# Kernel optimization log

Hardware: AMD Instinct MI355X
Metric: run time of the kernel (lower is better)

The kernel has to match this reference:

```python
import jax, jax.numpy as jnp
import numpy as np

B, S, H, GLU, VOC, L, CIN, BLK = 8, 256, 512, 1024, 256, 24, 320, 16
EPS = 1e-5


def setup_inputs() -> dict:
    key = jax.random.key(0)
    ks = jax.random.split(key, 16)
    r = lambda k, shp, s=0.02: (jax.random.normal(k, shp) * s).astype(jnp.float32)
    return {
        "x": jax.random.normal(ks[0], (B, CIN, 1, S), dtype=jnp.float32),
        "stem_w": r(ks[1], (H, CIN)),
        "rms_local": jnp.ones((L, H), jnp.float32),
        "rms_global": jnp.ones((L, H), jnp.float32),
        "rms_ffn": jnp.ones((L, H), jnp.float32),
        # alphas init to 0.0 in the torch module; use small nonzero values so
        # all sublayers actually contribute to the output / gradients.
        "alpha_local": (jax.random.normal(ks[2], (L,)) * 0.1).astype(jnp.float32),
        "alpha_global": (jax.random.normal(ks[3], (L,)) * 0.1).astype(jnp.float32),
        "alpha_mlp": (jax.random.normal(ks[4], (L,)) * 0.1).astype(jnp.float32),
        "w_local": r(ks[5], (L, H, BLK, BLK), 0.06),   # per-channel 16x16 mixing mats
        "w_global": r(ks[6], (L, H, BLK, BLK), 0.06),
        "wv": r(ks[7], (L, GLU, H)),
        "wg": r(ks[8], (L, GLU, H)),
        "wo": r(ks[9], (L, H, GLU)),
        "head_rms": jnp.ones((H,), jnp.float32),
        "head_logit_scale": jnp.float32(1.0),
        "head_w": r(ks[10], (VOC, H)),
    }


def _rmsnorm(h, w):
    # h: [B,C,S], w: [C]; mean-of-squares over channel axis (C == HIDDEN == 512)
    ms = jnp.mean(h * h, axis=1, keepdims=True)
    return h * jax.lax.rsqrt(ms + EPS) * w[None, :, None]


def _forward(x, stem_w, rms_local, rms_global, rms_ffn, alpha_local, alpha_global,
             alpha_mlp, w_local, w_global, wv, wg, wo, head_rms, head_logit_scale, head_w):
    h = jnp.einsum('oc,bcs->bos', stem_w, x[:, :, 0, :])  # stem conv1x1 -> [B,H,S]
    params = (rms_local, rms_global, rms_ffn, alpha_local, alpha_global, alpha_mlp,
              w_local, w_global, wv, wg, wo)

    def step(h, p):
        rl, rg, rf, al, ag, am, Wl, Wg, Wv, Wgt, Wo = p
        # s = i*16 + j : i = chunk index, j = within-chunk position
        u = _rmsnorm(h, rl).reshape(B, H, BLK, BLK)
        h = h + al * jnp.einsum('cpj,bcij->bcip', Wl, u).reshape(B, H, S)   # local: mix j
        v = _rmsnorm(h, rg).reshape(B, H, BLK, BLK)
        h = h + ag * jnp.einsum('cpi,bcij->bcpj', Wg, v).reshape(B, H, S)   # global: mix i
        w_ = _rmsnorm(h, rf)
        h1 = jnp.einsum('oc,bcs->bos', Wv, w_)
        h3 = jnp.einsum('oc,bcs->bos', Wgt, w_)
        h = h + am * jnp.einsum('co,bos->bcs', Wo, jax.nn.silu(h1) * h3)    # GLU MLP
        return h, None

    h, _ = jax.lax.scan(step, h, params)
    n = _rmsnorm(h, head_rms)
    logits = head_logit_scale * jnp.einsum('vc,bcs->bvs', head_w, n)
    return logits[:, :, None, :]  # [B, VOCAB, 1, S]


def reference(x, stem_w, rms_local, rms_global, rms_ffn, alpha_local, alpha_global,
              alpha_mlp, w_local, w_global, wv, wg, wo, head_rms, head_logit_scale, head_w):
    return _forward(x, stem_w, rms_local, rms_global, rms_ffn, alpha_local, alpha_global,
                    alpha_mlp, w_local, w_global, wv, wg, wo, head_rms,
                    head_logit_scale, head_w)
```

## Files before the change

kernel.cpp:

```cpp
#include <hip/hip_runtime.h>
#include <hip/hip_bf16.h>
#include <stdint.h>

#define NB 8
#define NS 256
#define NH 512
#define NG 1024
#define NV 256
#define NL 24
#define NC 320
#define NT 2048
#define EPSF 1e-5f

typedef __bf16 bf16;
typedef bf16 bf16x8 __attribute__((ext_vector_type(8)));
typedef float f32x4 __attribute__((ext_vector_type(4)));

__device__ __forceinline__ bf16 f2bf(float f) {
    uint32_t u = __builtin_bit_cast(uint32_t, f);
    u += 0x7FFFu + ((u >> 16) & 1u);
    uint16_t b = (uint16_t)(u >> 16);
    return __builtin_bit_cast(bf16, b);
}
__device__ __forceinline__ uint16_t bfbits(float f) {
    uint32_t u = __builtin_bit_cast(uint32_t, f);
    u += 0x7FFFu + ((u >> 16) & 1u);
    return (uint16_t)(u >> 16);
}

__device__ __forceinline__ void gload16(const void* g, void* l) {
    __builtin_amdgcn_global_load_lds(
        (const __attribute__((address_space(1))) void*)g,
        (__attribute__((address_space(3))) void*)l,
        16, 0, 0);
}

__device__ __forceinline__ void stage64(
    const bf16* __restrict__ src, int ldk, bf16* lds, int wv_, int lane)
{
    #pragma unroll
    for (int j = 0; j < 2; ++j) {
        const int gI = wv_*2 + j;
        const int r  = gI*8 + (lane >> 3);
        const int ch = (lane & 7) ^ (lane >> 3);
        gload16(src + (size_t)r*ldk + ch*8, lds + gI*512);
    }
}
__device__ __forceinline__ const bf16x8* fragp(const bf16* lds, int row, int ch) {
    return (const bf16x8*)(lds + row*64 + ((ch ^ (row & 7)) << 3));
}

#define MFMA(a,b,c) __builtin_amdgcn_mfma_f32_16x16x32_bf16(a, b, c, 0, 0, 0)

__global__ __launch_bounds__(256) void k_cvt(
    const float* __restrict__ src, bf16* __restrict__ dst, int n8)
{
    int i = blockIdx.x*256 + threadIdx.x;
    const int stride = gridDim.x*256;
    for (; i < n8; i += stride) {
        const float* sp = src + (size_t)i*8;
        float4 v0 = *(const float4*)&sp[0];
        float4 v1 = *(const float4*)&sp[4];
        bf16x8 t;
        t[0] = f2bf(v0.x); t[1] = f2bf(v0.y); t[2] = f2bf(v0.z); t[3] = f2bf(v0.w);
        t[4] = f2bf(v1.x); t[5] = f2bf(v1.y); t[6] = f2bf(v1.z); t[7] = f2bf(v1.w);
        *(bf16x8*)&dst[(size_t)i*8] = t;
    }
}

__global__ __launch_bounds__(256) void k_cvt2(
    const float* __restrict__ s0, const float* __restrict__ s1,
    bf16* __restrict__ d0, bf16* __restrict__ d1, int n8a, int n8b)
{
    const int N = n8a + n8b;
    for (int i = blockIdx.x*256 + threadIdx.x; i < N; i += gridDim.x*256) {
        const float* s; bf16* d; int j;
        if (i < n8a) { s = s0; d = d0; j = i; }
        else         { s = s1; d = d1; j = i - n8a; }
        const float* sp = s + (size_t)j*8;
        float4 v0 = *(const float4*)&sp[0];
        float4 v1 = *(const float4*)&sp[4];
        bf16x8 t;
        t[0] = f2bf(v0.x); t[1] = f2bf(v0.y); t[2] = f2bf(v0.z); t[3] = f2bf(v0.w);
        t[4] = f2bf(v1.x); t[5] = f2bf(v1.y); t[6] = f2bf(v1.z); t[7] = f2bf(v1.w);
        *(bf16x8*)&d[(size_t)j*8] = t;
    }
}

__global__ __launch_bounds__(256) void k_trw(
    const float* __restrict__ wl, const float* __restrict__ wg,
    bf16* __restrict__ wlT, bf16* __restrict__ wgT)
{
    __shared__ bf16 Ls[64*72];
    const int pj0 = blockIdx.x*64, c0 = blockIdx.y*64;
    const int z = blockIdx.z, l = z >> 1;
    const float* src = (z & 1) ? wg : wl;
    bf16* dst = (z & 1) ? wgT : wlT;
    src += (size_t)l*NH*256;
    dst += (size_t)l*256*NH;
    const int tid = threadIdx.x;
    #pragma unroll
    for (int e = 0; e < 16; ++e) {
        int idx = e*256 + tid;
        int cl = idx >> 6, pj = idx & 63;
        Ls[pj*72 + cl] = f2bf(src[(size_t)(c0 + cl)*256 + pj0 + pj]);
    }
    __syncthreads();
    #pragma unroll
    for (int e = 0; e < 2; ++e) {
        int idx = e*256 + tid;
        int row = idx >> 3, ch8 = idx & 7;
        *(bf16x8*)&dst[(size_t)(pj0 + row)*NH + c0 + ch8*8] =
            *(const bf16x8*)&Ls[row*72 + ch8*8];
    }
}

__global__ __launch_bounds__(256) void k_trx(
    const float* __restrict__ x, bf16* __restrict__ xT)
{
    __shared__ bf16 Ls[64*72];
    const int s0 = blockIdx.x*64, c0 = blockIdx.y*64, b = blockIdx.z;
    const int tid = threadIdx.x;
    #pragma unroll
    for (int e = 0; e < 16; ++e) {
        int idx = tid + e*256;
        int c = idx >> 6, s = idx & 63;
        Ls[s*72 + c] = f2bf(x[(size_t)(b*NC + c0 + c)*NS + s0 + s]);
    }
    __syncthreads();
    #pragma unroll
    for (int e = 0; e < 2; ++e) {
        int idx = tid + e*256;
        int s = idx >> 3, ch = idx & 7;
        *(bf16x8*)&xT[(size_t)(b*NS + s0 + s)*NC + c0 + ch*8] =
            *(const bf16x8*)&Ls[s*72 + ch*8];
    }
}

__global__ __launch_bounds__(256) void k_stem_b(
    const bf16* __restrict__ xT, const bf16* __restrict__ wb,
    float* __restrict__ h)
{
    __shared__ __align__(16) bf16 As[2][4096], Bs[2][4096];
    __shared__ float Cs[64*66];
    const int t0 = blockIdx.x*64, n0 = blockIdx.y*64;
    const int tid = threadIdx.x, lane = tid & 63, wv_ = tid >> 6;
    const int wm = wv_ >> 1, wn = wv_ & 1;
    const int fr = lane & 15, kq = lane >> 4;
    const bf16* Ag = xT + (size_t)t0*NC;
    const bf16* Bg = wb + (size_t)n0*NC;
    f32x4 acc[2][2] = {};
    stage64(Ag, NC, As[0], wv_, lane);
    stage64(Bg, NC, Bs[0], wv_, lane);
    __syncthreads();
    const int NIT = NC/64;
    for (int it = 0; it < NIT; ++it) {
        const int cur = it & 1;
        if (it + 1 < NIT) {
            stage64(Ag + (it+1)*64, NC, As[cur^1], wv_, lane);
            stage64(Bg + (it+1)*64, NC, Bs[cur^1], wv_, lane);
        }
        #pragma unroll
        for (int kk = 0; kk < 2; ++kk) {
            const int ch = kk*4 + kq;
            bf16x8 a0 = *fragp(As[cur], wm*32 + fr,      ch);
            bf16x8 a1 = *fragp(As[cur], wm*32 + 16 + fr, ch);
            bf16x8 b0 = *fragp(Bs[cur], wn*32 + fr,      ch);
            bf16x8 b1 = *fragp(Bs[cur], wn*32 + 16 + fr, ch);
            acc[0][0] = MFMA(a0, b0, acc[0][0]);
            acc[0][1] = MFMA(a0, b1, acc[0][1]);
            acc[1][0] = MFMA(a1, b0, acc[1][0]);
            acc[1][1] = MFMA(a1, b1, acc[1][1]);
        }
        __syncthreads();
    }
    const int row4 = (lane >> 4)*4, col = lane & 15;
    #pragma unroll
    for (int mi = 0; mi < 2; ++mi)
      #pragma unroll
      for (int ni = 0; ni < 2; ++ni)
        #pragma unroll
        for (int r = 0; r < 4; ++r)
            Cs[(wm*32 + mi*16 + row4 + r)*66 + wn*32 + ni*16 + col] = acc[mi][ni][r];
    __syncthreads();
    const int rr = tid >> 2, c16 = (tid & 3)*16;
    float* dst = &h[(size_t)(t0 + rr)*NH + n0 + c16];
    #pragma unroll
    for (int i = 0; i < 16; ++i) dst[i] = Cs[rr*66 + c16 + i];
}

template<int STR, bool FFN>
__global__ __launch_bounds__(256) void k_mix2(
    float* __restrict__ h, const bf16* __restrict__ wT,
    const float* __restrict__ rmsw, const float* __restrict__ alpha_p,
    const float* __restrict__ rmsw_ffn, bf16* __restrict__ a_bf)
{
    __shared__ float raw[16][512];
    __shared__ float red[4][16];
    __shared__ float rstdL[16];
    const int b = blockIdx.x, gi = blockIdx.y, ph = blockIdx.z;
    const int base = b*NS + (STR == 1 ? gi*16 : gi);
    const int tid = threadIdx.x, lane = tid & 63, wid = tid >> 6;
    #pragma unroll
    for (int e = 0; e < 8; ++e) {
        int idx = e*256 + tid;
        int k = idx >> 7, c4 = idx & 127;
        *(float4*)&raw[k][c4*4] = *(const float4*)&h[(size_t)(base + k*STR)*NH + c4*4];
    }
    __syncthreads();
    const int c0 = tid*2;
    float u0[16], u1[16], part[16];
    #pragma unroll
    for (int k = 0; k < 16; ++k) {
        float A = raw[k][c0], B = raw[k][c0+1];
        u0[k] = A; u1[k] = B; part[k] = A*A + B*B;
    }
    #pragma unroll
    for (int m = 1; m < 64; m <<= 1)
        #pragma unroll
        for (int k = 0; k < 16; ++k) part[k] += __shfl_xor(part[k], m, 64);
    if (lane == 0) {
        #pragma unroll
        for (int k = 0; k < 16; ++k) red[wid][k] = part[k];
    }
    __syncthreads();
    if (tid < 16)
        rstdL[tid] = rsqrtf((red[0][tid]+red[1][tid]+red[2][tid]+red[3][tid])*(1.f/NH) + EPSF);
    __syncthreads();
    #pragma unroll
    for (int k = 0; k < 16; ++k) { u0[k] *= rstdL[k]; u1[k] *= rstdL[k]; }
    const float al = *alpha_p;
    const float rc0 = rmsw[c0]*al, rc1 = rmsw[c0+1]*al;
    const uint32_t* wrow = (const uint32_t*)wT + tid;
    float hn0[8], hn1[8];
    #pragma unroll
    for (int pp = 0; pp < 8; ++pp) {
        const int p = ph*8 + pp;
        float a0 = 0.f, a1 = 0.f;
        #pragma unroll
        for (int k = 0; k < 16; ++k) {
            uint32_t wz = wrow[(p*16 + k)*256];
            float w0 = __builtin_bit_cast(float, wz << 16);
            float w1 = __builtin_bit_cast(float, wz & 0xffff0000u);
            a0 += w0*u0[k]; a1 += w1*u1[k];
        }
        hn0[pp] = raw[p][c0]   + rc0*a0;
        hn1[pp] = raw[p][c0+1] + rc1*a1;
        float2 o; o.x = hn0[pp]; o.y = hn1[pp];
        *(float2*)&h[(size_t)(base + p*STR)*NH + c0] = o;
    }
    if constexpr (FFN) {
        float p2[8];
        #pragma unroll
        for (int pp = 0; pp < 8; ++pp) p2[pp] = hn0[pp]*hn0[pp] + hn1[pp]*hn1[pp];
        #pragma unroll
        for (int m = 1; m < 64; m <<= 1)
            #pragma unroll
            for (int pp = 0; pp < 8; ++pp) p2[pp] += __shfl_xor(p2[pp], m, 64);
        __syncthreads();
        if (lane == 0) {
            #pragma unroll
            for (int pp = 0; pp < 8; ++pp) red[wid][pp] = p2[pp];
        }
        __syncthreads();
        if (tid < 8)
            rstdL[tid] = rsqrtf((red[0][tid]+red[1][tid]+red[2][tid]+red[3][tid])*(1.f/NH) + EPSF);
        __syncthreads();
        const float rf0 = rmsw_ffn[c0], rf1 = rmsw_ffn[c0+1];
        #pragma unroll
        for (int pp = 0; pp < 8; ++pp) {
            const int p = ph*8 + pp;
            float r = rstdL[pp];
            uint32_t pk = ((uint32_t)bfbits(hn1[pp]*r*rf1) << 16) | bfbits(hn0[pp]*r*rf0);
            *(uint32_t*)&a_bf[(size_t)(base + p*STR)*NH + c0] = pk;
        }
    }
}

__global__ __launch_bounds__(256) void k_norm2(
    const float* __restrict__ h, const float* __restrict__ rmsw,
    bf16* __restrict__ a)
{
    const int t = blockIdx.x*4 + (threadIdx.x >> 6);
    const int lane = threadIdx.x & 63;
    const int c8 = lane*8;
    const float* src = &h[(size_t)t*NH + c8];
    float4 h0 = *(const float4*)&src[0];
    float4 h1 = *(const float4*)&src[4];
    float ss = h0.x*h0.x + h0.y*h0.y + h0.z*h0.z + h0.w*h0.w
             + h1.x*h1.x + h1.y*h1.y + h1.z*h1.z + h1.w*h1.w;
    #pragma unroll
    for (int m = 1; m < 64; m <<= 1) ss += __shfl_xor(ss, m, 64);
    const float rstd = rsqrtf(ss*(1.f/NH) + EPSF);
    float4 w0 = *(const float4*)&rmsw[c8];
    float4 w1 = *(const float4*)&rmsw[c8 + 4];
    bf16x8 o;
    o[0] = f2bf(h0.x*rstd*w0.x); o[1] = f2bf(h0.y*rstd*w0.y);
    o[2] = f2bf(h0.z*rstd*w0.z); o[3] = f2bf(h0.w*rstd*w0.w);
    o[4] = f2bf(h1.x*rstd*w1.x); o[5] = f2bf(h1.y*rstd*w1.y);
    o[6] = f2bf(h1.z*rstd*w1.z); o[7] = f2bf(h1.w*rstd*w1.w);
    *(bf16x8*)&a[(size_t)t*NH + c8] = o;
}

__global__ __launch_bounds__(256) void k_mlp_in(
    const bf16* __restrict__ a, const bf16* __restrict__ wvl,
    const bf16* __restrict__ wgl, bf16* __restrict__ g)
{
    __shared__ __align__(16) bf16 As[2][4096], B1s[2][4096], B3s[2][4096];
    __shared__ bf16 Gs[64*72];
    const int t0 = blockIdx.x*64, n0 = blockIdx.y*64;
    const int tid = threadIdx.x, lane = tid & 63, wv_ = tid >> 6;
    const int wm = wv_ >> 1, wn = wv_ & 1;
    const int fr = lane & 15, kq = lane >> 4;
    const bf16* Ag = a   + (size_t)t0*NH;
    const bf16* Vg = wvl + (size_t)n0*NH;
    const bf16* Gg = wgl + (size_t)n0*NH;
    f32x4 acc1[2][2] = {}, acc3[2][2] = {};
    stage64(Ag, NH, As[0],  wv_, lane);
    stage64(Vg, NH, B1s[0], wv_, lane);
    stage64(Gg, NH, B3s[0], wv_, lane);
    __syncthreads();
    const int NIT = NH/64;
    for (int it = 0; it < NIT; ++it) {
        const int cur = it & 1;
        if (it + 1 < NIT) {
            stage64(Ag + (it+1)*64, NH, As[cur^1],  wv_, lane);
            stage64(Vg + (it+1)*64, NH, B1s[cur^1], wv_, lane);
            stage64(Gg + (it+1)*64, NH, B3s[cur^1], wv_, lane);
        }
        #pragma unroll
        for (int kk = 0; kk < 2; ++kk) {
            const int ch = kk*4 + kq;
            bf16x8 a0 = *fragp(As[cur],  wm*32 + fr,      ch);
            bf16x8 a1 = *fragp(As[cur],  wm*32 + 16 + fr, ch);
            bf16x8 u0 = *fragp(B1s[cur], wn*32 + fr,      ch);
            bf16x8 u1 = *fragp(B1s[cur], wn*32 + 16 + fr, ch);
            bf16x8 v0 = *fragp(B3s[cur], wn*32 + fr,      ch);
            bf16x8 v1 = *fragp(B3s[cur], wn*32 + 16 + fr, ch);
            acc1[0][0] = MFMA(a0, u0, acc1[0][0]);
            acc1[0][1] = MFMA(a0, u1, acc1[0][1]);
            acc1[1][0] = MFMA(a1, u0, acc1[1][0]);
            acc1[1][1] = MFMA(a1, u1, acc1[1][1]);
            acc3[0][0] = MFMA(a0, v0, acc3[0][0]);
            acc3[0][1] = MFMA(a0, v1, acc3[0][1]);
            acc3[1][0] = MFMA(a1, v0, acc3[1][0]);
            acc3[1][1] = MFMA(a1, v1, acc3[1][1]);
        }
        __syncthreads();
    }
    const int row4 = (lane >> 4)*4, col = lane & 15;
    #pragma unroll
    for (int mi = 0; mi < 2; ++mi)
      #pragma unroll
      for (int ni = 0; ni < 2; ++ni)
        #pragma unroll
        for (int r = 0; r < 4; ++r) {
            float xv = acc1[mi][ni][r];
            float gl = (xv / (1.f + __expf(-xv))) * acc3[mi][ni][r];
            Gs[(wm*32 + mi*16 + row4 + r)*72 + wn*32 + ni*16 + col] = f2bf(gl);
        }
    __syncthreads();
    const int rr = tid >> 2, c16 = (tid & 3)*16;
    bf16x8 o0 = *(const bf16x8*)&Gs[rr*72 + c16];
    bf16x8 o1 = *(const bf16x8*)&Gs[rr*72 + c16 + 8];
    *(bf16x8*)&g[(size_t)(t0 + rr)*NG + n0 + c16] = o0;
    *(bf16x8*)&g[(size_t)(t0 + rr)*NG + n0 + c16 + 8] = o1;
}

__global__ __launch_bounds__(256) void k_mlp_out(
    const bf16* __restrict__ g, const bf16* __restrict__ wol,
    const float* __restrict__ alpha_p, float* __restrict__ h)
{
    __shared__ __align__(16) bf16 As[2][4096], Bs[2][4096];
    __shared__ float Cs[64*66];
    const int t0 = blockIdx.x*64, n0 = blockIdx.y*64;
    const int tid = threadIdx.x, lane = tid & 63, wv_ = tid >> 6;
    const int wm = wv_ >> 1, wn = wv_ & 1;
    const int fr = lane & 15, kq = lane >> 4;
    const bf16* Ag = g   + (size_t)t0*NG;
    const bf16* Bg = wol + (size_t)n0*NG;
    f32x4 acc[2][2] = {};
    stage64(Ag, NG, As[0], wv_, lane);
    stage64(Bg, NG, Bs[0], wv_, lane);
    __syncthreads();
    const int NIT = NG/64;
    for (int it = 0; it < NIT; ++it) {
        const int cur = it & 1;
        if (it + 1 < NIT) {
            stage64(Ag + (it+1)*64, NG, As[cur^1], wv_, lane);
            stage64(Bg + (it+1)*64, NG, Bs[cur^1], wv_, lane);
        }
        #pragma unroll
        for (int kk = 0; kk < 2; ++kk) {
            const int ch = kk*4 + kq;
            bf16x8 a0 = *fragp(As[cur], wm*32 + fr,      ch);
            bf16x8 a1 = *fragp(As[cur], wm*32 + 16 + fr, ch);
            bf16x8 b0 = *fragp(Bs[cur], wn*32 + fr,      ch);
            bf16x8 b1 = *fragp(Bs[cur], wn*32 + 16 + fr, ch);
            acc[0][0] = MFMA(a0, b0, acc[0][0]);
            acc[0][1] = MFMA(a0, b1, acc[0][1]);
            acc[1][0] = MFMA(a1, b0, acc[1][0]);
            acc[1][1] = MFMA(a1, b1, acc[1][1]);
        }
        __syncthreads();
    }
    const int row4 = (lane >> 4)*4, col = lane & 15;
    #pragma unroll
    for (int mi = 0; mi < 2; ++mi)
      #pragma unroll
      for (int ni = 0; ni < 2; ++ni)
        #pragma unroll
        for (int r = 0; r < 4; ++r)
            Cs[(wm*32 + mi*16 + row4 + r)*66 + wn*32 + ni*16 + col] = acc[mi][ni][r];
    __syncthreads();
    const float am = *alpha_p;
    const int rr = tid >> 2, c16 = (tid & 3)*16;
    float* dst = &h[(size_t)(t0 + rr)*NH + n0 + c16];
    #pragma unroll
    for (int i = 0; i < 16; ++i)
        dst[i] = dst[i] + am * Cs[rr*66 + c16 + i];
}

__global__ __launch_bounds__(256) void k_head(
    const bf16* __restrict__ a, const bf16* __restrict__ hw,
    const float* __restrict__ scale_p, float* __restrict__ out)
{
    __shared__ __align__(16) bf16 As[2][4096], Bs[2][4096];
    __shared__ float Ls[64*66];
    const int t0 = blockIdx.x*64, n0 = blockIdx.y*64;
    const int tid = threadIdx.x, lane = tid & 63, wv_ = tid >> 6;
    const int wm = wv_ >> 1, wn = wv_ & 1;
    const int fr = lane & 15, kq = lane >> 4;
    const bf16* Ag = a  + (size_t)t0*NH;
    const bf16* Bg = hw + (size_t)n0*NH;
    f32x4 acc[2][2] = {};
    stage64(Ag, NH, As[0], wv_, lane);
    stage64(Bg, NH, Bs[0], wv_, lane);
    __syncthreads();
    const int NIT = NH/64;
    for (int it = 0; it < NIT; ++it) {
        const int cur = it & 1;
        if (it + 1 < NIT) {
            stage64(Ag + (it+1)*64, NH, As[cur^1], wv_, lane);
            stage64(Bg + (it+1)*64, NH, Bs[cur^1], wv_, lane);
        }
        #pragma unroll
        for (int kk = 0; kk < 2; ++kk) {
            const int ch = kk*4 + kq;
            bf16x8 a0 = *fragp(As[cur], wm*32 + fr,      ch);
            bf16x8 a1 = *fragp(As[cur], wm*32 + 16 + fr, ch);
            bf16x8 b0 = *fragp(Bs[cur], wn*32 + fr,      ch);
            bf16x8 b1 = *fragp(Bs[cur], wn*32 + 16 + fr, ch);
            acc[0][0] = MFMA(a0, b0, acc[0][0]);
            acc[0][1] = MFMA(a0, b1, acc[0][1]);
            acc[1][0] = MFMA(a1, b0, acc[1][0]);
            acc[1][1] = MFMA(a1, b1, acc[1][1]);
        }
        __syncthreads();
    }
    const float sc = *scale_p;
    const int row4 = (lane >> 4)*4, col = lane & 15;
    #pragma unroll
    for (int mi = 0; mi < 2; ++mi)
      #pragma unroll
      for (int ni = 0; ni < 2; ++ni)
        #pragma unroll
        for (int r = 0; r < 4; ++r)
            Ls[(wm*32 + mi*16 + row4 + r)*66 + wn*32 + ni*16 + col] = sc * acc[mi][ni][r];
    __syncthreads();
    const int vv = tid >> 2, s16 = (tid & 3)*16;
    const int b = t0 >> 8, s0 = t0 & 255;
    float* dst = &out[((size_t)(b*NV + n0 + vv))*NS + s0 + s16];
    #pragma unroll
    for (int i = 0; i < 16; ++i) dst[i] = Ls[(s16 + i)*66 + vv];
}

extern "C" void kernel_launch(void* const* d_in, const int* in_sizes, int n_in,
                              void* d_out, int out_size, void* d_ws, size_t ws_size,
                              hipStream_t stream) {
    const float* x          = (const float*)d_in[0];
    const float* stem_w     = (const float*)d_in[1];
    const float* rms_local  = (const float*)d_in[2];
    const float* rms_global = (const float*)d_in[3];
    const float* rms_ffn    = (const float*)d_in[4];
    const float* alpha_local  = (const float*)d_in[5];
    const float* alpha_global = (const float*)d_in[6];
    const float* alpha_mlp    = (const float*)d_in[7];
    const float* w_local    = (const float*)d_in[8];
    const float* w_global   = (const float*)d_in[9];
    const float* wv         = (const float*)d_in[10];
    const float* wg         = (const float*)d_in[11];
    const float* wo         = (const float*)d_in[12];
    const float* head_rms   = (const float*)d_in[13];
    const float* head_scale = (const float*)d_in[14];
    const float* head_w     = (const float*)d_in[15];
    float* out = (float*)d_out;

    char* ws = (char*)d_ws;
    const size_t MB = 1024*1024;
    float* h    = (float*)(ws);
    bf16*  g    = (bf16*)(ws + 4*MB);
    bf16*  a_bf = (bf16*)(ws + 8*MB);
    bf16* xT      = (bf16*)(ws + 16*MB);
    bf16* stem_wb = (bf16*)(ws + 18*MB);
    bf16* head_wb = (bf16*)(ws + 19*MB);
    bf16* wlT     = (bf16*)(ws + 20*MB);
    bf16* wgT     = (bf16*)(ws + 26*MB);
    bf16* wv_b    = (bf16*)(ws + 32*MB);
    bf16* wg_b    = (bf16*)(ws + 56*MB);
    bf16* wo_b    = (bf16*)(ws + 80*MB);

    k_cvt<<<2048, 256, 0, stream>>>(wv, wv_b, NL*NG*NH/8);
    k_cvt<<<2048, 256, 0, stream>>>(wg, wg_b, NL*NG*NH/8);
    k_cvt<<<2048, 256, 0, stream>>>(wo, wo_b, NL*NH*NG/8);
    k_cvt2<<<160, 256, 0, stream>>>(stem_w, head_w, stem_wb, head_wb,
                                    NH*NC/8, NV*NH/8);
    k_trw<<<dim3(4, 8, 48), 256, 0, stream>>>(w_local, w_global, wlT, wgT);
    k_trx<<<dim3(4, 5, 8), 256, 0, stream>>>(x, xT);

    k_stem_b<<<dim3(32, 8), 256, 0, stream>>>(xT, stem_wb, h);

    for (int l = 0; l < NL; ++l) {
        k_mix2<1, false><<<dim3(NB, 16, 2), 256, 0, stream>>>(
            h, wlT + (size_t)l*256*NH, rms_local + l*NH, alpha_local + l,
            nullptr, nullptr);
        k_mix2<16, true><<<dim3(NB, 16, 2), 256, 0, stream>>>(
            h, wgT + (size_t)l*256*NH, rms_global + l*NH, alpha_global + l,
            rms_ffn + l*NH, a_bf);
        k_mlp_in<<<dim3(32, 16), 256, 0, stream>>>(
            a_bf, wv_b + (size_t)l*NG*NH, wg_b + (size_t)l*NG*NH, g);
        k_mlp_out<<<dim3(32, 8), 256, 0, stream>>>(
            g, wo_b + (size_t)l*NH*NG, alpha_mlp + l, h);
    }
    k_norm2<<<512, 256, 0, stream>>>(h, head_rms, a_bf);
    k_head<<<dim3(32, 4), 256, 0, stream>>>(a_bf, head_wb, head_scale, out);
}
```

Before: 1.235 ms.

## Fuse MLP output projection with next layer's local block-mix

Adds a k_fuse kernel that computes the Wo projection and residual add for 16 tokens per block, keeps the updated rows in shared memory, then applies the next layer's RMSnorm and local 16x16 mixing before writing h. This removes one kernel launch and one full read/write of h per layer for 23 of the 24 layers. The trade-off is that the fused kernel uses only 128 blocks with a simple unpipelined MFMA loop, which may leave the GPU under-occupied compared with the separate mlp_out kernel.

```diff
diff --git a/kernel.cpp b/kernel.cpp
--- a/kernel.cpp
+++ b/kernel.cpp
@@ -273,6 +273,93 @@
             float r = rstdL[pp];
             uint32_t pk = ((uint32_t)bfbits(hn1[pp]*r*rf1) << 16) | bfbits(hn0[pp]*r*rf0);
             *(uint32_t*)&a_bf[(size_t)(base + p*STR)*NH + c0] = pk;
+        }
+    }
+}
+
+__global__ __launch_bounds__(512) void k_fuse(
+    const bf16* __restrict__ g, const bf16* __restrict__ wol,
+    const float* __restrict__ alpha_mlp_p, float* __restrict__ h,
+    const bf16* __restrict__ wT_next, const float* __restrict__ rms_next,
+    const float* __restrict__ alpha_loc_next)
+{
+    __shared__ float Cs[16][516];
+    __shared__ float rstdL[16];
+    const int tid = threadIdx.x, lane = tid & 63, w = tid >> 6;
+    const int t0 = blockIdx.x * 16;
+    const int fr = lane & 15, kq = lane >> 4;
+    f32x4 acc[4] = {};
+    const bf16* Ap = g   + (size_t)(t0 + fr)*NG + kq*8;
+    const bf16* Bp = wol + (size_t)(w*64 + fr)*NG + kq*8;
+    for (int k0 = 0; k0 < NG; k0 += 32) {
+        bf16x8 aF = *(const bf16x8*)(Ap + k0);
+        #pragma unroll
+        for (int f = 0; f < 4; ++f) {
+            bf16x8 bF = *(const bf16x8*)(Bp + (size_t)f*16*NG + k0);
+            acc[f] = MFMA(aF, bF, acc[f]);
+        }
+    }
+    const int row4 = (lane >> 4)*4, col = lane & 15;
+    #pragma unroll
+    for (int f = 0; f < 4; ++f)
+      #pragma unroll
+      for (int r = 0; r < 4; ++r)
+        Cs[row4 + r][w*64 + f*16 + col] = acc[f][r];
+    __syncthreads();
+    const float am = *alpha_mlp_p;
+    {
+        const int tk = tid >> 5, cs = (tid & 31)*16;
+        #pragma unroll
+        for (int j = 0; j < 4; ++j) {
+            float4 hv = *(const float4*)&h[(size_t)(t0 + tk)*NH + cs + j*4];
+            float4 cv = *(float4*)&Cs[tk][cs + j*4];
+            cv.x = hv.x + am*cv.x; cv.y = hv.y + am*cv.y;
+            cv.z = hv.z + am*cv.z; cv.w = hv.w + am*cv.w;
+            *(float4*)&Cs[tk][cs + j*4] = cv;
+        }
+    }
+    __syncthreads();
+    {
+        const int tk = tid >> 5, cs = (tid & 31)*16;
+        float ssum = 0.f;
+        #pragma unroll
+        for (int j = 0; j < 16; ++j) {
+            float v = Cs[tk][cs + j];
+            ssum += v*v;
+        }
+        ssum += __shfl_xor(ssum, 1, 64);
+        ssum += __shfl_xor(ssum, 2, 64);
+        ssum += __shfl_xor(ssum, 4, 64);
+        ssum += __shfl_xor(ssum, 8, 64);
+        ssum += __shfl_xor(ssum, 16, 64);
+        if ((tid & 31) == 0) rstdL[tk] = rsqrtf(ssum*(1.f/NH) + EPSF);
+    }
+    __syncthreads();
+    if (tid < 256) {
+        const int c0 = tid*2;
+        float u0[16], u1[16];
+        #pragma unroll
+        for (int k = 0; k < 16; ++k) {
+            u0[k] = Cs[k][c0]   * rstdL[k];
+            u1[k] = Cs[k][c0+1] * rstdL[k];
+        }
+        const float al = *alpha_loc_next;
+        const float rc0 = rms_next[c0]*al, rc1 = rms_next[c0+1]*al;
+        const uint32_t* wrow = (const uint32_t*)wT_next + tid;
+        #pragma unroll
+        for (int p = 0; p < 16; ++p) {
+            float a0 = 0.f, a1 = 0.f;
+            #pragma unroll
+            for (int k = 0; k < 16; ++k) {
+                uint32_t wz = wrow[(p*16 + k)*256];
+                float w0 = __builtin_bit_cast(float, wz << 16);
+                float w1 = __builtin_bit_cast(float, wz & 0xffff0000u);
+                a0 += w0*u0[k]; a1 += w1*u1[k];
+            }
+            float2 o;
+            o.x = Cs[p][c0]   + rc0*a0;
+            o.y = Cs[p][c0+1] + rc1*a1;
+            *(float2*)&h[(size_t)(t0 + p)*NH + c0] = o;
         }
     }
 }
@@ -519,18 +606,24 @@
     k_trx<<<dim3(4, 5, 8), 256, 0, stream>>>(x, xT);
 
     k_stem_b<<<dim3(32, 8), 256, 0, stream>>>(xT, stem_wb, h);
+    k_mix2<1, false><<<dim3(NB, 16, 2), 256, 0, stream>>>(
+        h, wlT, rms_local, alpha_local, nullptr, nullptr);
 
     for (int l = 0; l < NL; ++l) {
-        k_mix2<1, false><<<dim3(NB, 16, 2), 256, 0, stream>>>(
-            h, wlT + (size_t)l*256*NH, rms_local + l*NH, alpha_local + l,
-            nullptr, nullptr);
         k_mix2<16, true><<<dim3(NB, 16, 2), 256, 0, stream>>>(
             h, wgT + (size_t)l*256*NH, rms_global + l*NH, alpha_global + l,
             rms_ffn + l*NH, a_bf);
         k_mlp_in<<<dim3(32, 16), 256, 0, stream>>>(
             a_bf, wv_b + (size_t)l*NG*NH, wg_b + (size_t)l*NG*NH, g);
-        k_mlp_out<<<dim3(32, 8), 256, 0, stream>>>(
-            g, wo_b + (size_t)l*NH*NG, alpha_mlp + l, h);
+        if (l < NL-1) {
+            k_fuse<<<128, 512, 0, stream>>>(
+                g, wo_b + (size_t)l*NH*NG, alpha_mlp + l, h,
+                wlT + (size_t)(l+1)*256*NH, rms_local + (l+1)*NH,
+                alpha_local + (l+1));
+        } else {
+            k_mlp_out<<<dim3(32, 8), 256, 0, stream>>>(
+                g, wo_b + (size_t)l*NH*NG, alpha_mlp + l, h);
+        }
     }
     k_norm2<<<512, 256, 0, stream>>>(h, head_rms, a_bf);
     k_head<<<dim3(32, 4), 256, 0, stream>>>(a_bf, head_wb, head_scale, out);
```

After: 1.762 ms. +42.6%, slower.
